# Kernel tuning notes

Hardware: AMD Instinct MI355X
Metric: run time of the kernel (lower is better)

Reference implementation:

```python
import jax, jax.numpy as jnp
from jax import lax
import numpy as np

B, T, I, H = 8192, 365, 3, 34


def setup_inputs() -> dict:
    key = jax.random.key(0)
    ks = jax.random.split(key, 7)
    s_in = 1.0 / np.sqrt(I)
    s_h = 1.0 / np.sqrt(H)
    return {
        "x": jax.random.normal(ks[0], (B, T, I), dtype=jnp.float32),
        "fc0_w": jax.random.uniform(ks[1], (H, I), jnp.float32, -s_in, s_in),
        "fc0_b": jax.random.uniform(ks[2], (H,), jnp.float32, -s_in, s_in),
        "w_ih": jax.random.uniform(ks[3], (4 * H, H), jnp.float32, -s_h, s_h),
        "w_hh": jax.random.uniform(ks[4], (4 * H, H), jnp.float32, -s_h, s_h),
        "b_ih": jax.random.uniform(ks[5], (4 * H,), jnp.float32, -s_h, s_h),
        "b_hh": jax.random.uniform(ks[6], (4 * H,), jnp.float32, -s_h, s_h),
    }


def reference(x, fc0_w, fc0_b, w_ih, w_hh, b_ih, b_hh):
    # fc0: [B,T,I] -> [B,T,H]
    l1 = jnp.einsum("bti,hi->bth", x, fc0_w) + fc0_b
    # Precompute input-side gate projections for all timesteps: [B,T,4H]
    gx = jnp.einsum("bth,gh->btg", l1, w_ih) + b_ih + b_hh
    gx_t = jnp.swapaxes(gx, 0, 1)  # [T,B,4H]

    h0 = jnp.zeros((x.shape[0], fc0_w.shape[0]), dtype=x.dtype)
    c0 = h0

    def step(carry, g_t):
        h, c = carry
        gates = g_t + h @ w_hh.T  # [B,4H]
        i, f, g, o = jnp.split(gates, 4, axis=-1)  # torch gate order: i,f,g,o
        i = jax.nn.sigmoid(i)
        f = jax.nn.sigmoid(f)
        g = jnp.tanh(g)
        o = jax.nn.sigmoid(o)
        c_new = f * c + i * g
        h_new = o * jnp.tanh(c_new)
        return (h_new, c_new), h_new

    (_, _), hs = lax.scan(step, (h0, c0), gx_t)  # hs: [T,B,H]
    return jnp.swapaxes(hs, 0, 1)  # [B,T,H]
```

## Files before the change

kernel.cpp:

```cpp
#include <hip/hip_runtime.h>

namespace {

constexpr int Bn = 8192;
constexpr int Tn = 365;
constexpr int Hn = 34;
constexpr int GB = 16;
constexpr int KP = 104;

constexpr float L2E = 1.44269504088896340736f;

typedef __attribute__((ext_vector_type(8))) short bf16x8;
typedef __attribute__((ext_vector_type(4))) float f32x4;

__device__ __forceinline__ float fexp2(float v) { return __builtin_amdgcn_exp2f(v); }
__device__ __forceinline__ float frcp(float v)  { return __builtin_amdgcn_rcpf(v); }

__device__ __forceinline__ unsigned short f2bf(float f) {
    union { float f; unsigned u; } v; v.f = f;
    unsigned r = v.u + 0x7fffu + ((v.u >> 16) & 1u);
    return (unsigned short)(r >> 16);
}
__device__ __forceinline__ float bf2f(unsigned short s) {
    union { unsigned u; float f; } v; v.u = ((unsigned)s) << 16; return v.f;
}
__device__ __forceinline__ unsigned packh(float h) {
    unsigned short hh = f2bf(h);
    unsigned short hl = f2bf(h - bf2f(hh));
    return (unsigned)hh | ((unsigned)hl << 16);
}

__device__ __forceinline__ void block_sync_lds() {
    __builtin_amdgcn_sched_barrier(0);
    asm volatile("s_waitcnt lgkmcnt(0)" ::: "memory");
    __builtin_amdgcn_s_barrier();
    __builtin_amdgcn_sched_barrier(0);
}


__global__ __launch_bounds__(256) void lstm_kernel(
    const float* __restrict__ x,
    const float* __restrict__ fc0_w,
    const float* __restrict__ fc0_b,
    const float* __restrict__ w_ih,
    const float* __restrict__ w_hh,
    const float* __restrict__ b_ih,
    const float* __restrict__ b_hh,
    float* __restrict__ out)
{
    __shared__ __align__(16) unsigned short a_lds[2][GB][KP];

    const int tid  = threadIdx.x;
    const int lane = tid & 63;
    const int wv   = tid >> 6;
    const int b    = lane & 15;
    const int kg   = lane >> 4;

    const int nc   = (wv < 2) ? 9 : 8;
    const int base = (wv < 2) ? 9 * wv : 18 + 8 * (wv - 2);

    bf16x8 Wt[3][3];
    #pragma unroll
    for (int tau = 0; tau < 3; ++tau) {
        const int rhat = 16 * tau + b;
        const int jl = rhat >> 2, g = rhat & 3;
        const int r = (jl < nc) ? g * Hn + (base + jl) : -1;
        const float s = (g == 2) ? (2.f * L2E) : (-L2E);
        float wcv[3] = {0.f, 0.f, 0.f};
        float bia = 0.f;
        if (r >= 0) {
            float ab = 0.f;
            for (int m = 0; m < Hn; ++m) {
                const float wi = w_ih[r * Hn + m];
                wcv[0] += wi * fc0_w[m * 3 + 0];
                wcv[1] += wi * fc0_w[m * 3 + 1];
                wcv[2] += wi * fc0_w[m * 3 + 2];
                ab     += wi * fc0_b[m];
            }
            wcv[0] *= s; wcv[1] *= s; wcv[2] *= s;
            bia = s * (ab + b_ih[r] + b_hh[r]);
        }
        #pragma unroll
        for (int ks = 0; ks < 3; ++ks) {
            bf16x8 f;
            #pragma unroll
            for (int e = 0; e < 8; ++e) {
                const int k = ks * 32 + kg * 8 + e;
                float val = 0.f;
                if (r >= 0) {
                    if (k < 68)       val = s * w_hh[r * Hn + (k >> 1)];
                    else if (k < 71)  val = wcv[k - 68];
                    else if (k < 74)  val = wcv[k - 71];
                    else if (k < 77)  { const float w = wcv[k - 74]; val = w - bf2f(f2bf(w)); }
                    else if (k == 77) val = bia;
                    else if (k == 78) val = bia - bf2f(f2bf(bia));
                }
                f[e] = (short)f2bf(val);
            }
            Wt[tau][ks] = f;
        }
    }

    const bool has2 = (8 + kg < nc);
    float c0 = 0.f, c1 = 0.f, c2 = 0.f;
    float h0 = 0.f, h1 = 0.f, h2 = 0.f;

    const bool xact = (lane < 12);
    const int bx = 4 * wv + lane / 3;
    const int ix = lane - 3 * (lane / 3);

    for (int i = tid; i < 2 * GB * KP; i += 256) ((unsigned short*)a_lds)[i] = 0;
    block_sync_lds();

    const long long bg = (long long)blockIdx.x * GB;
    const float* xblk = x + bg * (long long)(Tn * 3);
    float* oblk = out + bg * (long long)(Tn * Hn);
    const long long TH = (long long)Tn * Hn;

    if (tid < 32) {
        a_lds[tid >> 4][tid & 15][77] = (unsigned short)0x3F80;
        a_lds[tid >> 4][tid & 15][78] = (unsigned short)0x3F80;
    }
    if (xact) {
        const float xr = xblk[bx * (Tn * 3) + ix];
        const unsigned short xh = f2bf(xr);
        a_lds[0][bx][68 + ix] = xh;
        a_lds[0][bx][71 + ix] = f2bf(xr - bf2f(xh));
        a_lds[0][bx][74 + ix] = xh;
    }
    block_sync_lds();

    for (int t = 0; t < Tn; ++t) {
        const int cur = t & 1, nxt = cur ^ 1;

        if (t) {
            const long long tb = (long long)b * TH + (long long)(t - 1) * Hn + base;
            oblk[tb + kg]     = h0;
            oblk[tb + 4 + kg] = h1;
            if (has2) oblk[tb + 8 + kg] = h2;
        }
        float xr = 0.f;
        if (xact && t + 1 < Tn)
            xr = xblk[bx * (Tn * 3) + (t + 1) * 3 + ix];

        bf16x8 av[3];
        #pragma unroll
        for (int ks = 0; ks < 3; ++ks)
            av[ks] = *(const bf16x8*)(&a_lds[cur][b][ks * 32 + kg * 8]);

        f32x4 acc[3];
        #pragma unroll
        for (int tau = 0; tau < 3; ++tau) {
            acc[tau] = f32x4{0.f, 0.f, 0.f, 0.f};
            #pragma unroll
            for (int ks = 0; ks < 3; ++ks)
                acc[tau] = __builtin_amdgcn_mfma_f32_16x16x32_bf16(Wt[tau][ks], av[ks], acc[tau], 0, 0, 0);
        }

        {
            const float gi = frcp(1.f + fexp2(acc[0][0]));
            const float gf = frcp(1.f + fexp2(acc[0][1]));
            const float gg = fmaf(-2.f, frcp(1.f + fexp2(acc[0][2])), 1.f);
            const float go = frcp(1.f + fexp2(acc[0][3]));
            c0 = gf * c0 + gi * gg;
            h0 = go * fmaf(-2.f, frcp(1.f + fexp2(c0 * (2.f * L2E))), 1.f);
            ((unsigned*)&a_lds[nxt][b][0])[base + kg] = packh(h0);
        }
        {
            const float gi = frcp(1.f + fexp2(acc[1][0]));
            const float gf = frcp(1.f + fexp2(acc[1][1]));
            const float gg = fmaf(-2.f, frcp(1.f + fexp2(acc[1][2])), 1.f);
            const float go = frcp(1.f + fexp2(acc[1][3]));
            c1 = gf * c1 + gi * gg;
            h1 = go * fmaf(-2.f, frcp(1.f + fexp2(c1 * (2.f * L2E))), 1.f);
            ((unsigned*)&a_lds[nxt][b][0])[base + 4 + kg] = packh(h1);
        }
        if (has2) {
            const float gi = frcp(1.f + fexp2(acc[2][0]));
            const float gf = frcp(1.f + fexp2(acc[2][1]));
            const float gg = fmaf(-2.f, frcp(1.f + fexp2(acc[2][2])), 1.f);
            const float go = frcp(1.f + fexp2(acc[2][3]));
            c2 = gf * c2 + gi * gg;
            h2 = go * fmaf(-2.f, frcp(1.f + fexp2(c2 * (2.f * L2E))), 1.f);
            ((unsigned*)&a_lds[nxt][b][0])[base + 8 + kg] = packh(h2);
        }

        if (xact) {
            const unsigned short xh = f2bf(xr);
            a_lds[nxt][bx][68 + ix] = xh;
            a_lds[nxt][bx][71 + ix] = f2bf(xr - bf2f(xh));
            a_lds[nxt][bx][74 + ix] = xh;
        }

        block_sync_lds();
    }

    {
        const long long tb = (long long)b * TH + (long long)(Tn - 1) * Hn + base;
        oblk[tb + kg]     = h0;
        oblk[tb + 4 + kg] = h1;
        if (has2) oblk[tb + 8 + kg] = h2;
    }
}

}

extern "C" void kernel_launch(void* const* d_in, const int* in_sizes, int n_in,
                              void* d_out, int out_size, void* d_ws, size_t ws_size,
                              hipStream_t stream) {
    const float* x     = (const float*)d_in[0];
    const float* fc0_w = (const float*)d_in[1];
    const float* fc0_b = (const float*)d_in[2];
    const float* w_ih  = (const float*)d_in[3];
    const float* w_hh  = (const float*)d_in[4];
    const float* b_ih  = (const float*)d_in[5];
    const float* b_hh  = (const float*)d_in[6];
    float* out = (float*)d_out;

    lstm_kernel<<<Bn / GB, 256, 0, stream>>>(x, fc0_w, fc0_b, w_ih, w_hh, b_ih, b_hh, out);
}
```

Baseline: 370.6 us.

## Split LSTM hidden units across nine waves, one MFMA tile each

Each block now runs 9 waves instead of 4, and each wave computes a single 16-row MFMA tile covering 4 hidden units instead of up to three tiles. This shortens the per-wave serial chain of MFMAs and transcendental gate math on every timestep of the recurrence. The last wave also loads x. The trade-off is more waves joining each per-step block barrier, one partially idle wave, and lower per-wave work.

```diff
diff --git a/kernel.cpp b/kernel.cpp
--- a/kernel.cpp
+++ b/kernel.cpp
@@ -6,6 +6,8 @@
 constexpr int Tn = 365;
 constexpr int Hn = 34;
 constexpr int GB = 16;
+constexpr int NW = 9;
+constexpr int NT = NW * 64;
 constexpr int KP = 104;
 
 constexpr float L2E = 1.44269504088896340736f;
@@ -38,7 +40,7 @@
 }
 
 
-__global__ __launch_bounds__(256) void lstm_kernel(
+__global__ __launch_bounds__(NT) void lstm_kernel(
     const float* __restrict__ x,
     const float* __restrict__ fc0_w,
     const float* __restrict__ fc0_b,
@@ -56,19 +58,16 @@
     const int b    = lane & 15;
     const int kg   = lane >> 4;
 
-    const int nc   = (wv < 2) ? 9 : 8;
-    const int base = (wv < 2) ? 9 * wv : 18 + 8 * (wv - 2);
-
-    bf16x8 Wt[3][3];
-    #pragma unroll
-    for (int tau = 0; tau < 3; ++tau) {
-        const int rhat = 16 * tau + b;
-        const int jl = rhat >> 2, g = rhat & 3;
-        const int r = (jl < nc) ? g * Hn + (base + jl) : -1;
+    bf16x8 Wt[3];
+    {
+        const int jl = 4 * wv + (b >> 2);
+        const int g  = b & 3;
+        const bool valid = (jl < Hn);
+        const int r = g * Hn + (valid ? jl : 0);
         const float s = (g == 2) ? (2.f * L2E) : (-L2E);
         float wcv[3] = {0.f, 0.f, 0.f};
         float bia = 0.f;
-        if (r >= 0) {
+        if (valid) {
             float ab = 0.f;
             for (int m = 0; m < Hn; ++m) {
                 const float wi = w_ih[r * Hn + m];
@@ -87,7 +86,7 @@
             for (int e = 0; e < 8; ++e) {
                 const int k = ks * 32 + kg * 8 + e;
                 float val = 0.f;
-                if (r >= 0) {
+                if (valid) {
                     if (k < 68)       val = s * w_hh[r * Hn + (k >> 1)];
                     else if (k < 71)  val = wcv[k - 68];
                     else if (k < 74)  val = wcv[k - 71];
@@ -97,19 +96,19 @@
                 }
                 f[e] = (short)f2bf(val);
             }
-            Wt[tau][ks] = f;
+            Wt[ks] = f;
         }
     }
 
-    const bool has2 = (8 + kg < nc);
-    float c0 = 0.f, c1 = 0.f, c2 = 0.f;
-    float h0 = 0.f, h1 = 0.f, h2 = 0.f;
+    const int j0 = 4 * wv + kg;
+    const bool jval = (j0 < Hn);
+    float c0 = 0.f, h0 = 0.f;
 
-    const bool xact = (lane < 12);
-    const int bx = 4 * wv + lane / 3;
-    const int ix = lane - 3 * (lane / 3);
+    const bool xact = (wv == 8) && (lane < 48);
+    const int bx = lane / 3;
+    const int ix = lane - 3 * bx;
 
-    for (int i = tid; i < 2 * GB * KP; i += 256) ((unsigned short*)a_lds)[i] = 0;
+    for (int i = tid; i < 2 * GB * KP; i += NT) ((unsigned short*)a_lds)[i] = 0;
     block_sync_lds();
 
     const long long bg = (long long)blockIdx.x * GB;
@@ -133,12 +132,8 @@
     for (int t = 0; t < Tn; ++t) {
         const int cur = t & 1, nxt = cur ^ 1;
 
-        if (t) {
-            const long long tb = (long long)b * TH + (long long)(t - 1) * Hn + base;
-            oblk[tb + kg]     = h0;
-            oblk[tb + 4 + kg] = h1;
-            if (has2) oblk[tb + 8 + kg] = h2;
-        }
+        if (t && jval)
+            oblk[(long long)b * TH + (long long)(t - 1) * Hn + j0] = h0;
         float xr = 0.f;
         if (xact && t + 1 < Tn)
             xr = xblk[bx * (Tn * 3) + (t + 1) * 3 + ix];
@@ -148,41 +143,19 @@
         for (int ks = 0; ks < 3; ++ks)
             av[ks] = *(const bf16x8*)(&a_lds[cur][b][ks * 32 + kg * 8]);
 
-        f32x4 acc[3];
+        f32x4 acc = {0.f, 0.f, 0.f, 0.f};
         #pragma unroll
-        for (int tau = 0; tau < 3; ++tau) {
-            acc[tau] = f32x4{0.f, 0.f, 0.f, 0.f};
-            #pragma unroll
-            for (int ks = 0; ks < 3; ++ks)
-                acc[tau] = __builtin_amdgcn_mfma_f32_16x16x32_bf16(Wt[tau][ks], av[ks], acc[tau], 0, 0, 0);
-        }
+        for (int ks = 0; ks < 3; ++ks)
+            acc = __builtin_amdgcn_mfma_f32_16x16x32_bf16(Wt[ks], av[ks], acc, 0, 0, 0);
 
-        {
-            const float gi = frcp(1.f + fexp2(acc[0][0]));
-            const float gf = frcp(1.f + fexp2(acc[0][1]));
-            const float gg = fmaf(-2.f, frcp(1.f + fexp2(acc[0][2])), 1.f);
-            const float go = frcp(1.f + fexp2(acc[0][3]));
+        if (jval) {
+            const float gi = frcp(1.f + fexp2(acc[0]));
+            const float gf = frcp(1.f + fexp2(acc[1]));
+            const float gg = fmaf(-2.f, frcp(1.f + fexp2(acc[2])), 1.f);
+            const float go = frcp(1.f + fexp2(acc[3]));
             c0 = gf * c0 + gi * gg;
             h0 = go * fmaf(-2.f, frcp(1.f + fexp2(c0 * (2.f * L2E))), 1.f);
-            ((unsigned*)&a_lds[nxt][b][0])[base + kg] = packh(h0);
-        }
-        {
-            const float gi = frcp(1.f + fexp2(acc[1][0]));
-            const float gf = frcp(1.f + fexp2(acc[1][1]));
-            const float gg = fmaf(-2.f, frcp(1.f + fexp2(acc[1][2])), 1.f);
-            const float go = frcp(1.f + fexp2(acc[1][3]));
-            c1 = gf * c1 + gi * gg;
-            h1 = go * fmaf(-2.f, frcp(1.f + fexp2(c1 * (2.f * L2E))), 1.f);
-            ((unsigned*)&a_lds[nxt][b][0])[base + 4 + kg] = packh(h1);
-        }
-        if (has2) {
-            const float gi = frcp(1.f + fexp2(acc[2][0]));
-            const float gf = frcp(1.f + fexp2(acc[2][1]));
-            const float gg = fmaf(-2.f, frcp(1.f + fexp2(acc[2][2])), 1.f);
-            const float go = frcp(1.f + fexp2(acc[2][3]));
-            c2 = gf * c2 + gi * gg;
-            h2 = go * fmaf(-2.f, frcp(1.f + fexp2(c2 * (2.f * L2E))), 1.f);
-            ((unsigned*)&a_lds[nxt][b][0])[base + 8 + kg] = packh(h2);
+            ((unsigned*)&a_lds[nxt][b][0])[j0] = packh(h0);
         }
 
         if (xact) {
@@ -195,12 +168,8 @@
         block_sync_lds();
     }
 
-    {
-        const long long tb = (long long)b * TH + (long long)(Tn - 1) * Hn + base;
-        oblk[tb + kg]     = h0;
-        oblk[tb + 4 + kg] = h1;
-        if (has2) oblk[tb + 8 + kg] = h2;
-    }
+    if (jval)
+        oblk[(long long)b * TH + (long long)(Tn - 1) * Hn + j0] = h0;
 }
 
 }
@@ -217,5 +186,5 @@
     const float* b_hh  = (const float*)d_in[6];
     float* out = (float*)d_out;
 
-    lstm_kernel<<<Bn / GB, 256, 0, stream>>>(x, fc0_w, fc0_b, w_ih, w_hh, b_ih, b_hh, out);
+    lstm_kernel<<<Bn / GB, NT, 0, stream>>>(x, fc0_w, fc0_b, w_ih, w_hh, b_ih, b_hh, out);
 }
```

Measured after the change: 371.7 us. Within noise of the previous version (+0.3%).
